# Kernel tuning notes

Measured on AMD Instinct MI355X. Metric: run time of the kernel, lower is better.

The kernel has to match this reference:

```python
import jax, jax.numpy as jnp
import numpy as np

EPS = 0.1
B, D, H = 1048576, 2, 64


def _lagrangian(xs, W0, b0, W1, b1, W2, b2, W3, b3):
    # xs: [2] single sample -> scalar Lagrangian L(q, v)
    h = jnp.tanh(xs @ W0 + b0)
    h = jnp.tanh(h @ W1 + b1)
    h = jnp.tanh(h @ W2 + b2)
    return (h @ W3 + b3)[0]


def setup_inputs() -> dict:
    key = jax.random.key(0)
    ks = jax.random.split(key, 9)
    def lin(k, fan_in, fan_out):
        # mimic nn.Linear default init U(-1/sqrt(fan_in), 1/sqrt(fan_in))
        bound = 1.0 / np.sqrt(fan_in)
        kw, kb = jax.random.split(k)
        W = jax.random.uniform(kw, (fan_in, fan_out), jnp.float32, -bound, bound)
        b = jax.random.uniform(kb, (fan_out,), jnp.float32, -bound, bound)
        return W, b
    W0, b0 = lin(ks[1], D, H)
    W1, b1 = lin(ks[2], H, H)
    W2, b2 = lin(ks[3], H, H)
    W3, b3 = lin(ks[4], H, 1)
    x = jax.random.normal(ks[0], (B, D), jnp.float32)
    return {"t": 0, "x": x, "W0": W0, "b0": b0, "W1": W1, "b1": b1,
            "W2": W2, "b2": b2, "W3": W3, "b3": b3}


def reference(t, x, W0, b0, W1, b1, W2, b2, W3, b3):
    lag = lambda xs: _lagrangian(xs, W0, b0, W1, b1, W2, b2, W3, b3)
    grad_all = jax.vmap(jax.grad(lag))(x)          # [B, 2]
    H_full = jax.vmap(jax.hessian(lag))(x)          # [B, 2, 2]
    dL_dq = grad_all[:, 0:1]                        # [B, 1]
    d2L_dqv = H_full[:, 1, 0:1]                     # d2L/(dv dq)
    d2L_dv2 = H_full[:, 1, 1:2]                     # d2L/dv2
    v = x[:, 1:2]
    a = (dL_dq - d2L_dqv * v) / (d2L_dv2 + EPS)
    return jnp.concatenate([v, a], axis=1)          # [B, 2]
```

## Files before the change

### kernel.cpp

```cpp
#include <hip/hip_runtime.h>
#include <hip/hip_fp16.h>

typedef _Float16 half8 __attribute__((ext_vector_type(8)));
typedef float    f32x4 __attribute__((ext_vector_type(4)));

#define EPSL 0.1f
#define LDSW 68
#define LDSW2 36

__device__ __forceinline__ float fast_tanh(float x) {
    float e = __expf(2.0f * x);
    return 1.0f - 2.0f * __builtin_amdgcn_rcpf(e + 1.0f);
}

__device__ __forceinline__ unsigned int pk2(float a, float b) {
    union { __fp16 __attribute__((ext_vector_type(2))) h; unsigned int u; } v;
    v.h = __builtin_amdgcn_cvt_pkrtz(a, b);
    return v.u;
}
__device__ __forceinline__ float2 unpk2(unsigned int u) {
    union { unsigned int u; __half2 h; } v; v.u = u;
    return __half22float2(v.h);
}

__global__ void pack_weights(const float* __restrict__ W1,
                             const float* __restrict__ W2,
                             _Float16* __restrict__ pk) {
    const int t = threadIdx.x;
    const int q = t >> 4, r = t & 15;
    for (int kt = 0; kt < 2; ++kt)
        for (int nt = 0; nt < 4; ++nt)
            for (int j = 0; j < 8; ++j) {
                const int k = kt * 32 + q * 8 + j;
                const int n = nt * 16 + r;
                const int base = ((kt * 4 + nt) * 64 + t) * 8 + j;
                pk[0 * 4096 + base] = (_Float16)W1[k * 64 + n];
                pk[1 * 4096 + base] = (_Float16)W2[k * 64 + n];
                pk[2 * 4096 + base] = (_Float16)W2[n * 64 + k];
                pk[3 * 4096 + base] = (_Float16)W1[n * 64 + k];
            }
}

extern "C" __global__ void __launch_bounds__(256, 4)
lnn_mfma(const float* __restrict__ x,
         const float* __restrict__ W0, const float* __restrict__ b0,
         const float* __restrict__ b1, const float* __restrict__ b2,
         const float* __restrict__ W3,
         const _Float16* __restrict__ pk,
         float* __restrict__ out)
{
    __shared__ unsigned int lds [64 * LDSW];
    __shared__ unsigned int lds2[64 * LDSW2];

    const int t    = threadIdx.x & 63;
    const int w    = threadIdx.x >> 6;
    const int q    = t >> 4;
    const int r    = t & 15;
    const int wrow = w * 16;
    const long sbase = (long)blockIdx.x * 64 + wrow;

    const float2 xv = *(const float2*)(x + 2 * (sbase + r));
    const float x0 = xv.x, x1 = xv.y;

    auto ldpk = [&](int mat, int kt, int nt) -> half8 {
        return *(const half8*)(pk + ((mat * 2 + kt) * 4 + nt) * 512 + t * 8);
    };
    auto ldfrag = [&](int row, int kt, half8& vf, half8& tf) {
        const int off = row * LDSW + kt * 32 + q * 8;
        const uint4 A = *(const uint4*)&lds[off];
        const uint4 B = *(const uint4*)&lds[off + 4];
        union { unsigned int u[4]; half8 h; } cv, ct;
        cv.u[0] = __builtin_amdgcn_perm(A.y, A.x, 0x05040100u);
        cv.u[1] = __builtin_amdgcn_perm(A.w, A.z, 0x05040100u);
        cv.u[2] = __builtin_amdgcn_perm(B.y, B.x, 0x05040100u);
        cv.u[3] = __builtin_amdgcn_perm(B.w, B.z, 0x05040100u);
        ct.u[0] = __builtin_amdgcn_perm(A.y, A.x, 0x07060302u);
        ct.u[1] = __builtin_amdgcn_perm(A.w, A.z, 0x07060302u);
        ct.u[2] = __builtin_amdgcn_perm(B.y, B.x, 0x07060302u);
        ct.u[3] = __builtin_amdgcn_perm(B.w, B.z, 0x07060302u);
        vf = cv.h; tf = ct.h;
    };

    half8 ah0[2], at0[2];
    #pragma unroll
    for (int kt = 0; kt < 2; ++kt) {
        const int f = kt * 32 + q * 8;
        const float4 waA = *(const float4*)(W0 + f);
        const float4 waB = *(const float4*)(W0 + f + 4);
        const float4 wbA = *(const float4*)(W0 + 64 + f);
        const float4 wbB = *(const float4*)(W0 + 64 + f + 4);
        const float4 bbA = *(const float4*)(b0 + f);
        const float4 bbB = *(const float4*)(b0 + f + 4);
        const float wa[8] = {waA.x, waA.y, waA.z, waA.w, waB.x, waB.y, waB.z, waB.w};
        const float wb[8] = {wbA.x, wbA.y, wbA.z, wbA.w, wbB.x, wbB.y, wbB.z, wbB.w};
        const float bb[8] = {bbA.x, bbA.y, bbA.z, bbA.w, bbB.x, bbB.y, bbB.z, bbB.w};
        float h0v[8], t0v[8];
        #pragma unroll
        for (int j = 0; j < 8; ++j) {
            const float z0 = fmaf(x0, wa[j], fmaf(x1, wb[j], bb[j]));
            const float h0 = fast_tanh(z0);
            h0v[j] = h0;
            t0v[j] = fmaf(-h0, h0, 1.0f) * wb[j];
        }
        union { unsigned int u[4]; half8 h; } ph, pt;
        #pragma unroll
        for (int p = 0; p < 4; ++p) {
            ph.u[p] = pk2(h0v[2 * p], h0v[2 * p + 1]);
            pt.u[p] = pk2(t0v[2 * p], t0v[2 * p + 1]);
        }
        *(uint4*)&lds2[(wrow + r) * LDSW2 + kt * 16 + q * 4] = *(const uint4*)ph.u;
        ah0[kt] = ph.h; at0[kt] = pt.h;
    }

    f32x4 acc[4], tacc[4];
    #pragma unroll
    for (int nt = 0; nt < 4; ++nt) { acc[nt] = (f32x4){0,0,0,0}; tacc[nt] = (f32x4){0,0,0,0}; }
    #pragma unroll
    for (int kt = 0; kt < 2; ++kt)
        #pragma unroll
        for (int nt = 0; nt < 4; ++nt) {
            const half8 bw = ldpk(0, kt, nt);
            acc[nt]  = __builtin_amdgcn_mfma_f32_16x16x32_f16(ah0[kt], bw, acc[nt], 0, 0, 0);
            tacc[nt] = __builtin_amdgcn_mfma_f32_16x16x32_f16(at0[kt], bw, tacc[nt], 0, 0, 0);
        }

    unsigned int h1p[4][4];
    #pragma unroll
    for (int nt = 0; nt < 4; ++nt) {
        const float b1f = b1[nt * 16 + r];
        #pragma unroll
        for (int g = 0; g < 4; ++g) {
            const float z1 = acc[nt][g] + b1f;
            const float h1 = fast_tanh(z1);
            const float th1 = fmaf(-h1, h1, 1.0f) * tacc[nt][g];
            const unsigned int u = pk2(h1, th1);
            h1p[nt][g] = u;
            lds[(wrow + q * 4 + g) * LDSW + nt * 16 + r] = u;
        }
    }
    __builtin_amdgcn_wave_barrier();

    #pragma unroll
    for (int nt = 0; nt < 4; ++nt) { acc[nt] = (f32x4){0,0,0,0}; tacc[nt] = (f32x4){0,0,0,0}; }
    #pragma unroll
    for (int kt = 0; kt < 2; ++kt) {
        half8 av, at;
        ldfrag(wrow + r, kt, av, at);
        #pragma unroll
        for (int nt = 0; nt < 4; ++nt) {
            const half8 bw = ldpk(1, kt, nt);
            acc[nt]  = __builtin_amdgcn_mfma_f32_16x16x32_f16(av, bw, acc[nt], 0, 0, 0);
            tacc[nt] = __builtin_amdgcn_mfma_f32_16x16x32_f16(at, bw, tacc[nt], 0, 0, 0);
        }
    }
    __builtin_amdgcn_wave_barrier();

    #pragma unroll
    for (int nt = 0; nt < 4; ++nt) {
        const float b2f = b2[nt * 16 + r];
        const float w3f = W3[nt * 16 + r];
        #pragma unroll
        for (int g = 0; g < 4; ++g) {
            const float z2 = acc[nt][g] + b2f;
            const float h2 = fast_tanh(z2);
            const float A2 = fmaf(-h2, h2, 1.0f);
            const float dz2 = w3f * A2;
            const float t1  = h2 * tacc[nt][g];
            const float td2 = -2.0f * (dz2 * t1);
            lds[(wrow + q * 4 + g) * LDSW + nt * 16 + r] = pk2(dz2, td2);
        }
    }
    __builtin_amdgcn_wave_barrier();

    #pragma unroll
    for (int nt = 0; nt < 4; ++nt) { acc[nt] = (f32x4){0,0,0,0}; tacc[nt] = (f32x4){0,0,0,0}; }
    #pragma unroll
    for (int kt = 0; kt < 2; ++kt) {
        half8 av, at;
        ldfrag(wrow + r, kt, av, at);
        #pragma unroll
        for (int nt = 0; nt < 4; ++nt) {
            const half8 bw = ldpk(2, kt, nt);
            acc[nt]  = __builtin_amdgcn_mfma_f32_16x16x32_f16(av, bw, acc[nt], 0, 0, 0);
            tacc[nt] = __builtin_amdgcn_mfma_f32_16x16x32_f16(at, bw, tacc[nt], 0, 0, 0);
        }
    }
    __builtin_amdgcn_wave_barrier();

    #pragma unroll
    for (int nt = 0; nt < 4; ++nt)
        #pragma unroll
        for (int g = 0; g < 4; ++g) {
            const float g1 = acc[nt][g];
            const float tg1 = tacc[nt][g];
            const float2 ht = unpk2(h1p[nt][g]);
            const float A1 = fmaf(-ht.x, ht.x, 1.0f);
            const float d1 = g1 * A1;
            const float u = g1 * ht.x * ht.y;
            const float td1 = fmaf(tg1, A1, -2.0f * u);
            lds[(wrow + q * 4 + g) * LDSW + nt * 16 + r] = pk2(d1, td1);
        }
    __builtin_amdgcn_wave_barrier();

    #pragma unroll
    for (int mt = 0; mt < 4; ++mt) { acc[mt] = (f32x4){0,0,0,0}; tacc[mt] = (f32x4){0,0,0,0}; }
    #pragma unroll
    for (int kt = 0; kt < 2; ++kt) {
        half8 bd, btd;
        ldfrag(wrow + r, kt, bd, btd);
        #pragma unroll
        for (int mt = 0; mt < 4; ++mt) {
            const half8 aw = ldpk(3, kt, mt);
            acc[mt]  = __builtin_amdgcn_mfma_f32_16x16x32_f16(aw, bd,  acc[mt], 0, 0, 0);
            tacc[mt] = __builtin_amdgcn_mfma_f32_16x16x32_f16(aw, btd, tacc[mt], 0, 0, 0);
        }
    }

    float pg = 0.f, ph0 = 0.f, ph1 = 0.f;
    #pragma unroll
    for (int mt = 0; mt < 4; ++mt) {
        const int f = mt * 16 + q * 4;
        const float4 waF = *(const float4*)(W0 + f);
        const float4 wbF = *(const float4*)(W0 + 64 + f);
        const float wa[4] = {waF.x, waF.y, waF.z, waF.w};
        const float wb[4] = {wbF.x, wbF.y, wbF.z, wbF.w};
        const uint2 hh = *(const uint2*)&lds2[(wrow + r) * LDSW2 + mt * 8 + q * 2];
        const float2 hA = unpk2(hh.x);
        const float2 hB = unpk2(hh.y);
        const float h0v[4] = {hA.x, hA.y, hB.x, hB.y};
        #pragma unroll
        for (int g = 0; g < 4; ++g) {
            const float h0 = h0v[g];
            const float A0 = fmaf(-h0, h0, 1.0f);
            const float th0 = A0 * wb[g];
            const float g0 = acc[mt][g];
            const float tg0 = tacc[mt][g];
            const float d0 = g0 * A0;
            const float u = g0 * h0 * th0;
            const float td0 = fmaf(-2.0f, u, tg0 * A0);
            pg  = fmaf(wa[g], d0, pg);
            ph0 = fmaf(wa[g], td0, ph0);
            ph1 = fmaf(wb[g], td0, ph1);
        }
    }
    pg  += __shfl_xor(pg, 16);  pg  += __shfl_xor(pg, 32);
    ph0 += __shfl_xor(ph0, 16); ph0 += __shfl_xor(ph0, 32);
    ph1 += __shfl_xor(ph1, 16); ph1 += __shfl_xor(ph1, 32);
    if (q == 0) {
        const float num = fmaf(-ph0, x1, pg);
        const float a = num / (ph1 + EPSL);
        float2 o;
        o.x = x1;
        o.y = a;
        *(float2*)(out + 2 * (sbase + r)) = o;
    }
}

extern "C" void kernel_launch(void* const* d_in, const int* in_sizes, int n_in,
                              void* d_out, int out_size, void* d_ws, size_t ws_size,
                              hipStream_t stream) {
    const float* x  = (const float*)d_in[1];
    const float* W0 = (const float*)d_in[2];
    const float* b0 = (const float*)d_in[3];
    const float* W1 = (const float*)d_in[4];
    const float* b1 = (const float*)d_in[5];
    const float* W2 = (const float*)d_in[6];
    const float* b2 = (const float*)d_in[7];
    const float* W3 = (const float*)d_in[8];

    _Float16* pk = (_Float16*)d_ws;
    const int B = in_sizes[1] / 2;

    pack_weights<<<1, 64, 0, stream>>>(W1, W2, pk);
    lnn_mfma<<<B / 64, 256, 0, stream>>>(x, W0, b0, b1, b2, W3, pk, (float*)d_out);
}
```

Before: 217.7 us.

## Vectorize elementwise math to packed f32x2, fold biases, parallelize weight packing

Rewrites the per-element tanh and derivative math to operate on float2 vectors so the compiler can emit packed FP32 instructions (v_pk_fma/mul). It uses exp2 with a pre-scaled argument instead of expf, folds the b1/b2 biases into the MFMA accumulator initial value, and replaces the final division with a reciprocal. The weight-packing kernel now spreads its work over 32 blocks with vector stores instead of a single block. Together these aim to cut VALU instruction count in a kernel dominated by elementwise work, and to shorten the serial pack launch. The rcp-based division adds a small accuracy change.

```diff
diff --git a/kernel.cpp b/kernel.cpp
--- a/kernel.cpp
+++ b/kernel.cpp
@@ -3,14 +3,28 @@
 
 typedef _Float16 half8 __attribute__((ext_vector_type(8)));
 typedef float    f32x4 __attribute__((ext_vector_type(4)));
+typedef float    f32x2 __attribute__((ext_vector_type(2)));
 
 #define EPSL 0.1f
 #define LDSW 68
 #define LDSW2 36
-
-__device__ __forceinline__ float fast_tanh(float x) {
-    float e = __expf(2.0f * x);
-    return 1.0f - 2.0f * __builtin_amdgcn_rcpf(e + 1.0f);
+#define TWO_LOG2E 2.8853900817779268f
+
+#if __has_builtin(__builtin_amdgcn_exp2f)
+#define EXP2(x) __builtin_amdgcn_exp2f(x)
+#else
+#define EXP2(x) __expf((x) * 0.6931471805599453f)
+#endif
+
+__device__ __forceinline__ f32x2 tanh2s(f32x2 y) {
+    f32x2 e;
+    e.x = EXP2(y.x);
+    e.y = EXP2(y.y);
+    const f32x2 ep = e + 1.0f;
+    f32x2 r;
+    r.x = __builtin_amdgcn_rcpf(ep.x);
+    r.y = __builtin_amdgcn_rcpf(ep.y);
+    return 1.0f - 2.0f * r;
 }
 
 __device__ __forceinline__ unsigned int pk2(float a, float b) {
@@ -18,27 +32,36 @@
     v.h = __builtin_amdgcn_cvt_pkrtz(a, b);
     return v.u;
 }
-__device__ __forceinline__ float2 unpk2(unsigned int u) {
+__device__ __forceinline__ f32x2 unpk2v(unsigned int u) {
     union { unsigned int u; __half2 h; } v; v.u = u;
-    return __half22float2(v.h);
-}
+    const float2 f = __half22float2(v.h);
+    return (f32x2){f.x, f.y};
+}
+__device__ __forceinline__ f32x2 lo2(f32x4 v) { return __builtin_shufflevector(v, v, 0, 1); }
+__device__ __forceinline__ f32x2 hi2(f32x4 v) { return __builtin_shufflevector(v, v, 2, 3); }
 
 __global__ void pack_weights(const float* __restrict__ W1,
                              const float* __restrict__ W2,
                              _Float16* __restrict__ pk) {
     const int t = threadIdx.x;
+    const int combo = blockIdx.x;
+    const int nt  = combo & 3;
+    const int kt  = (combo >> 2) & 1;
+    const int mat = combo >> 3;
     const int q = t >> 4, r = t & 15;
-    for (int kt = 0; kt < 2; ++kt)
-        for (int nt = 0; nt < 4; ++nt)
-            for (int j = 0; j < 8; ++j) {
-                const int k = kt * 32 + q * 8 + j;
-                const int n = nt * 16 + r;
-                const int base = ((kt * 4 + nt) * 64 + t) * 8 + j;
-                pk[0 * 4096 + base] = (_Float16)W1[k * 64 + n];
-                pk[1 * 4096 + base] = (_Float16)W2[k * 64 + n];
-                pk[2 * 4096 + base] = (_Float16)W2[n * 64 + k];
-                pk[3 * 4096 + base] = (_Float16)W1[n * 64 + k];
-            }
+    const int n = nt * 16 + r;
+    _Float16 v[8];
+    #pragma unroll
+    for (int j = 0; j < 8; ++j) {
+        const int k = kt * 32 + q * 8 + j;
+        float x;
+        if (mat == 0)      x = W1[k * 64 + n];
+        else if (mat == 1) x = W2[k * 64 + n];
+        else if (mat == 2) x = W2[n * 64 + k];
+        else               x = W1[n * 64 + k];
+        v[j] = (_Float16)x;
+    }
+    *(half8*)(pk + combo * 512 + t * 8) = *(const half8*)v;
 }
 
 extern "C" __global__ void __launch_bounds__(256, 4)
@@ -91,22 +114,18 @@
         const float4 wbB = *(const float4*)(W0 + 64 + f + 4);
         const float4 bbA = *(const float4*)(b0 + f);
         const float4 bbB = *(const float4*)(b0 + f + 4);
-        const float wa[8] = {waA.x, waA.y, waA.z, waA.w, waB.x, waB.y, waB.z, waB.w};
-        const float wb[8] = {wbA.x, wbA.y, wbA.z, wbA.w, wbB.x, wbB.y, wbB.z, wbB.w};
-        const float bb[8] = {bbA.x, bbA.y, bbA.z, bbA.w, bbB.x, bbB.y, bbB.z, bbB.w};
-        float h0v[8], t0v[8];
-        #pragma unroll
-        for (int j = 0; j < 8; ++j) {
-            const float z0 = fmaf(x0, wa[j], fmaf(x1, wb[j], bb[j]));
-            const float h0 = fast_tanh(z0);
-            h0v[j] = h0;
-            t0v[j] = fmaf(-h0, h0, 1.0f) * wb[j];
-        }
+        const f32x2 wa2[4] = {{waA.x,waA.y},{waA.z,waA.w},{waB.x,waB.y},{waB.z,waB.w}};
+        const f32x2 wb2[4] = {{wbA.x,wbA.y},{wbA.z,wbA.w},{wbB.x,wbB.y},{wbB.z,wbB.w}};
+        const f32x2 bb2[4] = {{bbA.x,bbA.y},{bbA.z,bbA.w},{bbB.x,bbB.y},{bbB.z,bbB.w}};
         union { unsigned int u[4]; half8 h; } ph, pt;
         #pragma unroll
         for (int p = 0; p < 4; ++p) {
-            ph.u[p] = pk2(h0v[2 * p], h0v[2 * p + 1]);
-            pt.u[p] = pk2(t0v[2 * p], t0v[2 * p + 1]);
+            const f32x2 z = x0 * wa2[p] + x1 * wb2[p] + bb2[p];
+            const f32x2 h = tanh2s(z * TWO_LOG2E);
+            const f32x2 A = 1.0f - h * h;
+            const f32x2 tt = A * wb2[p];
+            ph.u[p] = pk2(h.x, h.y);
+            pt.u[p] = pk2(tt.x, tt.y);
         }
         *(uint4*)&lds2[(wrow + r) * LDSW2 + kt * 16 + q * 4] = *(const uint4*)ph.u;
         ah0[kt] = ph.h; at0[kt] = pt.h;
@@ -114,7 +133,11 @@
 
     f32x4 acc[4], tacc[4];
     #pragma unroll
-    for (int nt = 0; nt < 4; ++nt) { acc[nt] = (f32x4){0,0,0,0}; tacc[nt] = (f32x4){0,0,0,0}; }
+    for (int nt = 0; nt < 4; ++nt) {
+        const float bf = b1[nt * 16 + r];
+        acc[nt]  = (f32x4){bf, bf, bf, bf};
+        tacc[nt] = (f32x4){0, 0, 0, 0};
+    }
     #pragma unroll
     for (int kt = 0; kt < 2; ++kt)
         #pragma unroll
@@ -127,21 +150,29 @@
     unsigned int h1p[4][4];
     #pragma unroll
     for (int nt = 0; nt < 4; ++nt) {
-        const float b1f = b1[nt * 16 + r];
-        #pragma unroll
-        for (int g = 0; g < 4; ++g) {
-            const float z1 = acc[nt][g] + b1f;
-            const float h1 = fast_tanh(z1);
-            const float th1 = fmaf(-h1, h1, 1.0f) * tacc[nt][g];
-            const unsigned int u = pk2(h1, th1);
-            h1p[nt][g] = u;
-            lds[(wrow + q * 4 + g) * LDSW + nt * 16 + r] = u;
-        }
-    }
-    __builtin_amdgcn_wave_barrier();
-
-    #pragma unroll
-    for (int nt = 0; nt < 4; ++nt) { acc[nt] = (f32x4){0,0,0,0}; tacc[nt] = (f32x4){0,0,0,0}; }
+        const f32x2 zp[2] = {lo2(acc[nt]),  hi2(acc[nt])};
+        const f32x2 tp[2] = {lo2(tacc[nt]), hi2(tacc[nt])};
+        #pragma unroll
+        for (int p = 0; p < 2; ++p) {
+            const f32x2 h  = tanh2s(zp[p] * TWO_LOG2E);
+            const f32x2 A  = 1.0f - h * h;
+            const f32x2 th = A * tp[p];
+            const unsigned int u0 = pk2(h.x, th.x);
+            const unsigned int u1 = pk2(h.y, th.y);
+            h1p[nt][2 * p]     = u0;
+            h1p[nt][2 * p + 1] = u1;
+            lds[(wrow + q * 4 + 2 * p)     * LDSW + nt * 16 + r] = u0;
+            lds[(wrow + q * 4 + 2 * p + 1) * LDSW + nt * 16 + r] = u1;
+        }
+    }
+    __builtin_amdgcn_wave_barrier();
+
+    #pragma unroll
+    for (int nt = 0; nt < 4; ++nt) {
+        const float bf = b2[nt * 16 + r];
+        acc[nt]  = (f32x4){bf, bf, bf, bf};
+        tacc[nt] = (f32x4){0, 0, 0, 0};
+    }
     #pragma unroll
     for (int kt = 0; kt < 2; ++kt) {
         half8 av, at;
@@ -157,17 +188,18 @@
 
     #pragma unroll
     for (int nt = 0; nt < 4; ++nt) {
-        const float b2f = b2[nt * 16 + r];
         const float w3f = W3[nt * 16 + r];
-        #pragma unroll
-        for (int g = 0; g < 4; ++g) {
-            const float z2 = acc[nt][g] + b2f;
-            const float h2 = fast_tanh(z2);
-            const float A2 = fmaf(-h2, h2, 1.0f);
-            const float dz2 = w3f * A2;
-            const float t1  = h2 * tacc[nt][g];
-            const float td2 = -2.0f * (dz2 * t1);
-            lds[(wrow + q * 4 + g) * LDSW + nt * 16 + r] = pk2(dz2, td2);
+        const f32x2 zp[2] = {lo2(acc[nt]),  hi2(acc[nt])};
+        const f32x2 tp[2] = {lo2(tacc[nt]), hi2(tacc[nt])};
+        #pragma unroll
+        for (int p = 0; p < 2; ++p) {
+            const f32x2 h  = tanh2s(zp[p] * TWO_LOG2E);
+            const f32x2 A  = 1.0f - h * h;
+            const f32x2 dz = A * w3f;
+            const f32x2 t1 = h * tp[p];
+            const f32x2 td = -2.0f * (dz * t1);
+            lds[(wrow + q * 4 + 2 * p)     * LDSW + nt * 16 + r] = pk2(dz.x, td.x);
+            lds[(wrow + q * 4 + 2 * p + 1) * LDSW + nt * 16 + r] = pk2(dz.y, td.y);
         }
     }
     __builtin_amdgcn_wave_barrier();
@@ -188,18 +220,23 @@
     __builtin_amdgcn_wave_barrier();
 
     #pragma unroll
-    for (int nt = 0; nt < 4; ++nt)
-        #pragma unroll
-        for (int g = 0; g < 4; ++g) {
-            const float g1 = acc[nt][g];
-            const float tg1 = tacc[nt][g];
-            const float2 ht = unpk2(h1p[nt][g]);
-            const float A1 = fmaf(-ht.x, ht.x, 1.0f);
-            const float d1 = g1 * A1;
-            const float u = g1 * ht.x * ht.y;
-            const float td1 = fmaf(tg1, A1, -2.0f * u);
-            lds[(wrow + q * 4 + g) * LDSW + nt * 16 + r] = pk2(d1, td1);
-        }
+    for (int nt = 0; nt < 4; ++nt) {
+        const f32x2 gp[2] = {lo2(acc[nt]),  hi2(acc[nt])};
+        const f32x2 tp[2] = {lo2(tacc[nt]), hi2(tacc[nt])};
+        #pragma unroll
+        for (int p = 0; p < 2; ++p) {
+            const unsigned int hu = __builtin_amdgcn_perm(h1p[nt][2*p+1], h1p[nt][2*p], 0x05040100u);
+            const unsigned int tu = __builtin_amdgcn_perm(h1p[nt][2*p+1], h1p[nt][2*p], 0x07060302u);
+            const f32x2 h  = unpk2v(hu);
+            const f32x2 th = unpk2v(tu);
+            const f32x2 A  = 1.0f - h * h;
+            const f32x2 d1 = gp[p] * A;
+            const f32x2 u2 = (gp[p] * h) * th;
+            const f32x2 td = tp[p] * A + (-2.0f) * u2;
+            lds[(wrow + q * 4 + 2 * p)     * LDSW + nt * 16 + r] = pk2(d1.x, td.x);
+            lds[(wrow + q * 4 + 2 * p + 1) * LDSW + nt * 16 + r] = pk2(d1.y, td.y);
+        }
+    }
     __builtin_amdgcn_wave_barrier();
 
     #pragma unroll
@@ -216,39 +253,41 @@
         }
     }
 
-    float pg = 0.f, ph0 = 0.f, ph1 = 0.f;
+    f32x2 pg2 = {0, 0}, ph02 = {0, 0}, ph12 = {0, 0};
     #pragma unroll
     for (int mt = 0; mt < 4; ++mt) {
         const int f = mt * 16 + q * 4;
         const float4 waF = *(const float4*)(W0 + f);
         const float4 wbF = *(const float4*)(W0 + 64 + f);
-        const float wa[4] = {waF.x, waF.y, waF.z, waF.w};
-        const float wb[4] = {wbF.x, wbF.y, wbF.z, wbF.w};
+        const f32x2 wa2[2] = {{waF.x, waF.y}, {waF.z, waF.w}};
+        const f32x2 wb2[2] = {{wbF.x, wbF.y}, {wbF.z, wbF.w}};
         const uint2 hh = *(const uint2*)&lds2[(wrow + r) * LDSW2 + mt * 8 + q * 2];
-        const float2 hA = unpk2(hh.x);
-        const float2 hB = unpk2(hh.y);
-        const float h0v[4] = {hA.x, hA.y, hB.x, hB.y};
-        #pragma unroll
-        for (int g = 0; g < 4; ++g) {
-            const float h0 = h0v[g];
-            const float A0 = fmaf(-h0, h0, 1.0f);
-            const float th0 = A0 * wb[g];
-            const float g0 = acc[mt][g];
-            const float tg0 = tacc[mt][g];
-            const float d0 = g0 * A0;
-            const float u = g0 * h0 * th0;
-            const float td0 = fmaf(-2.0f, u, tg0 * A0);
-            pg  = fmaf(wa[g], d0, pg);
-            ph0 = fmaf(wa[g], td0, ph0);
-            ph1 = fmaf(wb[g], td0, ph1);
-        }
-    }
+        const unsigned int hu[2] = {hh.x, hh.y};
+        const f32x2 gp[2] = {lo2(acc[mt]),  hi2(acc[mt])};
+        const f32x2 tp[2] = {lo2(tacc[mt]), hi2(tacc[mt])};
+        #pragma unroll
+        for (int p = 0; p < 2; ++p) {
+            const f32x2 h   = unpk2v(hu[p]);
+            const f32x2 A   = 1.0f - h * h;
+            const f32x2 th0 = A * wb2[p];
+            const f32x2 d0  = gp[p] * A;
+            const f32x2 u2  = (gp[p] * h) * th0;
+            const f32x2 td0 = tp[p] * A + (-2.0f) * u2;
+            pg2  += wa2[p] * d0;
+            ph02 += wa2[p] * td0;
+            ph12 += wb2[p] * td0;
+        }
+    }
+    float pg  = pg2.x  + pg2.y;
+    float ph0 = ph02.x + ph02.y;
+    float ph1 = ph12.x + ph12.y;
     pg  += __shfl_xor(pg, 16);  pg  += __shfl_xor(pg, 32);
     ph0 += __shfl_xor(ph0, 16); ph0 += __shfl_xor(ph0, 32);
     ph1 += __shfl_xor(ph1, 16); ph1 += __shfl_xor(ph1, 32);
     if (q == 0) {
         const float num = fmaf(-ph0, x1, pg);
-        const float a = num / (ph1 + EPSL);
+        const float den = ph1 + EPSL;
+        const float a = num * __builtin_amdgcn_rcpf(den);
         float2 o;
         o.x = x1;
         o.y = a;
@@ -271,6 +310,6 @@
     _Float16* pk = (_Float16*)d_ws;
     const int B = in_sizes[1] / 2;
 
-    pack_weights<<<1, 64, 0, stream>>>(W1, W2, pk);
+    pack_weights<<<32, 64, 0, stream>>>(W1, W2, pk);
     lnn_mfma<<<B / 64, 256, 0, stream>>>(x, W0, b0, b1, b2, W3, pk, (float*)d_out);
 }
```

After: 218.6 us. No clear change (+0.4%).
